# Performance work log

Hardware: AMD Instinct MI355X
Metric: run time of the kernel (lower is better)

Reference implementation:

```python
import jax, jax.numpy as jnp
import numpy as np

N_NODES = 100000
D_EMB = 128          # per-node embedding dim; concat dim = 2*D_EMB = 256
HIDDEN = 64
N_EDGES = 300000


def setup_inputs() -> dict:
    key = jax.random.key(0)
    ks = jax.random.split(key, 8)
    src_embs = jax.random.normal(ks[0], (N_NODES, D_EMB), dtype=jnp.float32)
    dst_embs = jax.random.normal(ks[1], (N_NODES, D_EMB), dtype=jnp.float32)
    edges_src_ids = jax.random.randint(ks[2], (N_EDGES,), 0, N_NODES, dtype=jnp.int64)
    edges_dst_ids = jax.random.randint(ks[3], (N_EDGES,), 0, N_NODES, dtype=jnp.int64)
    # elayers = Linear(256, 64) -> ReLU -> Linear(64, 1)
    s1 = 1.0 / np.sqrt(2 * D_EMB)
    s2 = 1.0 / np.sqrt(HIDDEN)
    W1 = jax.random.uniform(ks[4], (2 * D_EMB, HIDDEN), jnp.float32, -s1, s1)
    b1 = jax.random.uniform(ks[5], (HIDDEN,), jnp.float32, -s1, s1)
    W2 = jax.random.uniform(ks[6], (HIDDEN, 1), jnp.float32, -s2, s2)
    b2 = jax.random.uniform(ks[7], (1,), jnp.float32, -s2, s2)
    return {
        "src_embs": src_embs,
        "dst_embs": dst_embs,
        "edges_src_ids": edges_src_ids,
        "edges_dst_ids": edges_dst_ids,
        "W1": W1,
        "b1": b1,
        "W2": W2,
        "b2": b2,
    }


def reference(src_embs, dst_embs, edges_src_ids, edges_dst_ids, W1, b1, W2, b2):
    # Gather per-edge endpoint embeddings and concatenate: [E, 2*D]
    edge_feats = jnp.concatenate(
        [src_embs[edges_src_ids], dst_embs[edges_dst_ids]], axis=1
    )
    # Linear -> ReLU -> Linear, producing one logit per edge: [E, 1]
    h = jax.nn.relu(edge_feats @ W1 + b1)
    edge_logits = h @ W2 + b2
    return edge_logits
```

## Files before the change

kernel.cpp:

```cpp
#include <hip/hip_runtime.h>
#include <hip/hip_bf16.h>

typedef float f32x4 __attribute__((ext_vector_type(4)));
typedef __bf16 bf16x8 __attribute__((ext_vector_type(8)));
typedef __bf16 bf16x4 __attribute__((ext_vector_type(4)));

#define DEMB 128
#define HIDDEN 64
#define W1T_STRIDE 264

typedef const __attribute__((address_space(1))) void* gas_ptr;
typedef __attribute__((address_space(3))) void* las_ptr;

__global__ __launch_bounds__(256) void w1frag_kernel(
    const float* __restrict__ W1, __bf16* __restrict__ wsfrag)
{
    const int gid = blockIdx.x * 256 + threadIdx.x;
    if (gid >= 2048) return;
    const int tb  = gid >> 10;
    const int cid = gid & 1023;
    const int el = cid & 15;
    const int gk = (cid >> 4) & 3;
    const int kk = (cid >> 6) & 3;
    const int t  = (cid >> 8) & 3;
    const int kbase = tb * 128 + kk * 32 + gk * 8;
    bf16x8 ch;
#pragma unroll
    for (int j = 0; j < 8; ++j)
        ch[j] = (__bf16)W1[(kbase + j) * HIDDEN + 4 * el + t];
    *reinterpret_cast<bf16x8*>(wsfrag + (size_t)gid * 8) = ch;
}

__global__ __launch_bounds__(256) void node_part9_kernel(
    const float* __restrict__ src_embs,
    const float* __restrict__ dst_embs,
    const __bf16* __restrict__ wsfrag,
    __bf16* __restrict__ spart,
    __bf16* __restrict__ dpart,
    int n_tiles, int blocks_per_table)
{
    __shared__ __bf16 frag_lds[1024 * 8];
    __shared__ float  bounce[4][512];

    const int table = (blockIdx.x >= blocks_per_table) ? 1 : 0;
    const int bid = blockIdx.x - table * blocks_per_table;
    const float* __restrict__ E = table ? dst_embs : src_embs;
    __bf16* __restrict__ P = table ? dpart : spart;

    const int lane = threadIdx.x & 63;
    const int el = lane & 15;
    const int gk = lane >> 4;
    const int wid = threadIdx.x >> 6;

    {
        const char* src = (const char*)(wsfrag + (size_t)table * 1024 * 8);
#pragma unroll
        for (int r = 0; r < 4; ++r) {
            const int off = (wid * 4 + r) * 1024;
            __builtin_amdgcn_global_load_lds(
                (gas_ptr)(src + off + lane * 16),
                (las_ptr)((char*)frag_lds + off), 16, 0, 0);
        }
        asm volatile("s_waitcnt vmcnt(0)" ::: "memory");
    }
    __syncthreads();

    char* obc = (char*)&bounce[wid][0];
    const int tstride = blocks_per_table * 4;
    int tile = bid * 4 + wid;
    if (tile >= n_tiles) return;

    f32x4 Ra[8], Rb[8];

#define LOADT(T, R)                                                          \
    do {                                                                     \
        const float* rp_ = E + (size_t)(T) * 2048 + el * 128 + gk * 8;       \
        _Pragma("unroll")                                                    \
        for (int kk = 0; kk < 4; ++kk) {                                     \
            (R)[2 * kk]     = *reinterpret_cast<const f32x4*>(rp_ + kk * 32);\
            (R)[2 * kk + 1] = *reinterpret_cast<const f32x4*>(rp_ + kk * 32 + 4);\
        }                                                                    \
    } while (0)

#define COMPUTE_STORE(T, R)                                                  \
    do {                                                                     \
        f32x4 acc[4] = {{0.f,0.f,0.f,0.f},{0.f,0.f,0.f,0.f},                 \
                        {0.f,0.f,0.f,0.f},{0.f,0.f,0.f,0.f}};                \
        _Pragma("unroll")                                                    \
        for (int kk = 0; kk < 4; ++kk) {                                     \
            bf16x8 a;                                                        \
            _Pragma("unroll")                                                \
            for (int j = 0; j < 4; ++j) {                                    \
                a[j]     = (__bf16)(R)[2 * kk][j];                           \
                a[4 + j] = (__bf16)(R)[2 * kk + 1][j];                       \
            }                                                                \
            _Pragma("unroll")                                                \
            for (int t = 0; t < 4; ++t) {                                    \
                const bf16x8 b = *reinterpret_cast<const bf16x8*>(           \
                    &frag_lds[(size_t)((t * 4 + kk) * 4 + gk) * 128 + el * 8]);\
                acc[t] = __builtin_amdgcn_mfma_f32_16x16x32_bf16(a, b, acc[t], 0, 0, 0);\
            }                                                                \
        }                                                                    \
        _Pragma("unroll")                                                    \
        for (int r = 0; r < 4; ++r) {                                        \
            bf16x4 pk;                                                       \
            _Pragma("unroll")                                                \
            for (int t = 0; t < 4; ++t) pk[t] = (__bf16)acc[t][r];           \
            *reinterpret_cast<bf16x4*>(obc + (gk * 4 + r) * 128 + el * 8) = pk;\
        }                                                                    \
        asm volatile("s_waitcnt lgkmcnt(0)" ::: "memory");                   \
        f32x4 c0 = *reinterpret_cast<const f32x4*>(obc + lane * 32);         \
        f32x4 c1 = *reinterpret_cast<const f32x4*>(obc + lane * 32 + 16);    \
        char* pb = (char*)P + (size_t)(T) * 2048;                            \
        *reinterpret_cast<f32x4*>(pb + lane * 32) = c0;                      \
        *reinterpret_cast<f32x4*>(pb + lane * 32 + 16) = c1;                 \
    } while (0)

    LOADT(tile, Ra);
    bool useA = true;
    while (true) {
        const int nxt = tile + tstride;
        if (useA) {
            if (nxt < n_tiles) LOADT(nxt, Rb);
            __builtin_amdgcn_sched_barrier(0);
            COMPUTE_STORE(tile, Ra);
        } else {
            if (nxt < n_tiles) LOADT(nxt, Ra);
            __builtin_amdgcn_sched_barrier(0);
            COMPUTE_STORE(tile, Rb);
        }
        useA = !useA;
        tile = nxt;
        if (tile >= n_tiles) break;
    }
#undef LOADT
#undef COMPUTE_STORE
}

__global__ __launch_bounds__(256, 8) void edge_tail2_kernel(
    const __bf16* __restrict__ spart,
    const __bf16* __restrict__ dpart,
    const int* __restrict__ src_ids,
    const int* __restrict__ dst_ids,
    const float* __restrict__ b1,
    const float* __restrict__ W2,
    const float* __restrict__ b2,
    float* __restrict__ out,
    int n_edges)
{
    const int lane = threadIdx.x & 63;
    const int c = lane & 7;
    float b1v[8], w2v[8];
#pragma unroll
    for (int j = 0; j < 8; ++j) { b1v[j] = b1[c * 8 + j]; w2v[j] = W2[c * 8 + j]; }
    const float bias2 = b2[0];

    int gid = (blockIdx.x * blockDim.x + threadIdx.x) >> 3;
    const int gstride = (gridDim.x * blockDim.x) >> 3;

    for (int e = gid; e < n_edges; e += gstride) {
        const long long sid = src_ids[e];
        const long long did = dst_ids[e];
        const bf16x8 s8 = *reinterpret_cast<const bf16x8*>(spart + sid * HIDDEN + c * 8);
        const bf16x8 d8 = *reinterpret_cast<const bf16x8*>(dpart + did * HIDDEN + c * 8);
        float v = 0.f;
#pragma unroll
        for (int j = 0; j < 8; ++j) {
            float h = (float)s8[j] + (float)d8[j] + b1v[j];
            h = fmaxf(h, 0.f);
            v = fmaf(h, w2v[j], v);
        }
        v += __shfl_xor(v, 1, 64);
        v += __shfl_xor(v, 2, 64);
        v += __shfl_xor(v, 4, 64);
        if (c == 0) out[e] = v + bias2;
    }
}

__global__ __launch_bounds__(256) void edge_mlp_kernel(
    const float* __restrict__ src_embs,
    const float* __restrict__ dst_embs,
    const int* __restrict__ src_ids,
    const int* __restrict__ dst_ids,
    const float* __restrict__ W1,
    const float* __restrict__ b1,
    const float* __restrict__ W2,
    const float* __restrict__ b2,
    float* __restrict__ out,
    int n_edges, int n_groups)
{
    __shared__ __bf16 w1t[64 * W1T_STRIDE];
    for (int s = threadIdx.x; s < 256 * 64; s += 256) {
        int k = s >> 6;
        int n = s & 63;
        w1t[n * W1T_STRIDE + k] = (__bf16)W1[s];
    }
    __syncthreads();

    const int lane = threadIdx.x & 63;
    const int el = lane & 15;
    const int gk = lane >> 4;

    float b1v[4], w2v[4];
#pragma unroll
    for (int t = 0; t < 4; ++t) { b1v[t] = b1[16 * t + el]; w2v[t] = W2[16 * t + el]; }
    const float bias2 = b2[0];

    const int gw0 = blockIdx.x * 4 + (threadIdx.x >> 6);
    const int gstride = gridDim.x * 4;

    for (int g = gw0; g < n_groups; g += gstride) {
        const int e_base = g * 16;
        int e = e_base + el;
        if (e >= n_edges) e = n_edges - 1;
        const long long sid = src_ids[e];
        const long long did = dst_ids[e];
        const float* sp = src_embs + sid * DEMB + gk * 8;
        const float* dp = dst_embs + did * DEMB + gk * 8;

        f32x4 acc[4] = {{0.f,0.f,0.f,0.f},{0.f,0.f,0.f,0.f},
                        {0.f,0.f,0.f,0.f},{0.f,0.f,0.f,0.f}};
#pragma unroll
        for (int kk = 0; kk < 8; ++kk) {
            const float* ap = (kk < 4) ? (sp + kk * 32) : (dp + (kk - 4) * 32);
            f32x4 f0 = *reinterpret_cast<const f32x4*>(ap);
            f32x4 f1 = *reinterpret_cast<const f32x4*>(ap + 4);
            bf16x8 a;
#pragma unroll
            for (int j = 0; j < 4; ++j) { a[j] = (__bf16)f0[j]; a[4+j] = (__bf16)f1[j]; }
#pragma unroll
            for (int t = 0; t < 4; ++t) {
                const bf16x8 bfrag = *reinterpret_cast<const bf16x8*>(
                    &w1t[(16 * t + el) * W1T_STRIDE + kk * 32 + gk * 8]);
                acc[t] = __builtin_amdgcn_mfma_f32_16x16x32_bf16(a, bfrag, acc[t], 0, 0, 0);
            }
        }
        float s0[4];
#pragma unroll
        for (int r = 0; r < 4; ++r) {
            float v = 0.f;
#pragma unroll
            for (int t = 0; t < 4; ++t) {
                float h = acc[t][r] + b1v[t];
                h = fmaxf(h, 0.f);
                v = fmaf(h, w2v[t], v);
            }
#pragma unroll
            for (int m = 1; m < 16; m <<= 1) v += __shfl_xor(v, m, 64);
            s0[r] = v + bias2;
        }
        const int row0 = e_base + gk * 4;
        if (el == 0) {
            if (row0 + 4 <= n_edges) {
                f32x4 o = {s0[0], s0[1], s0[2], s0[3]};
                *reinterpret_cast<f32x4*>(out + row0) = o;
            } else {
#pragma unroll
                for (int r = 0; r < 4; ++r)
                    if (row0 + r < n_edges) out[row0 + r] = s0[r];
            }
        }
    }
}

extern "C" void kernel_launch(void* const* d_in, const int* in_sizes, int n_in,
                              void* d_out, int out_size, void* d_ws, size_t ws_size,
                              hipStream_t stream) {
    const float* src_embs = (const float*)d_in[0];
    const float* dst_embs = (const float*)d_in[1];
    const int*   src_ids  = (const int*)d_in[2];
    const int*   dst_ids  = (const int*)d_in[3];
    const float* W1 = (const float*)d_in[4];
    const float* b1 = (const float*)d_in[5];
    const float* W2 = (const float*)d_in[6];
    const float* b2 = (const float*)d_in[7];
    float* out = (float*)d_out;

    const int n_edges = in_sizes[2];
    const int n_nodes = in_sizes[0] / DEMB;
    const size_t part_elems = (size_t)n_nodes * HIDDEN;
    const size_t need = 2 * part_elems * sizeof(__bf16) + 32768;

    if (ws_size >= need && (n_nodes % 16) == 0) {
        __bf16* spart = (__bf16*)d_ws;
        __bf16* dpart = spart + part_elems;
        __bf16* wsfrag = dpart + part_elems;
        const int n_tiles = n_nodes / 16;

        w1frag_kernel<<<8, 256, 0, stream>>>(W1, wsfrag);

        int bpt = 384;
        if (bpt * 4 > n_tiles) bpt = (n_tiles + 3) / 4;
        node_part9_kernel<<<2 * bpt, 256, 0, stream>>>(
            src_embs, dst_embs, wsfrag, spart, dpart, n_tiles, bpt);

        int blocks2 = (n_edges + 31) / 32;
        if (blocks2 > 2048) blocks2 = 2048;
        edge_tail2_kernel<<<blocks2, 256, 0, stream>>>(
            spart, dpart, src_ids, dst_ids, b1, W2, b2, out, n_edges);
    } else {
        const int n_groups = (n_edges + 15) / 16;
        int blocks = (n_groups + 3) / 4;
        if (blocks > 1024) blocks = 1024;
        edge_mlp_kernel<<<blocks, 256, 0, stream>>>(
            src_embs, dst_embs, src_ids, dst_ids, W1, b1, W2, b2, out,
            n_edges, n_groups);
    }
}
```

Measured before the change: 43.34 us.

## Fuse W1 fragment prep into node kernel and triple-buffer tile loads

Removes the separate w1frag kernel launch: each block now converts its half of W1 to bf16 MFMA fragments directly into LDS. The node projection loop moves from double to triple buffering of embedding tiles, with out-of-range prefetches clamped to the last tile, and the grid drops from 384 to 256 blocks per table. This saves a launch and deepens prefetch, but every block now does redundant strided fp32 reads of W1, and the extra register buffer may lower occupancy.

```diff
diff --git a/kernel.cpp b/kernel.cpp
--- a/kernel.cpp
+++ b/kernel.cpp
@@ -9,32 +9,10 @@
 #define HIDDEN 64
 #define W1T_STRIDE 264
 
-typedef const __attribute__((address_space(1))) void* gas_ptr;
-typedef __attribute__((address_space(3))) void* las_ptr;
-
-__global__ __launch_bounds__(256) void w1frag_kernel(
-    const float* __restrict__ W1, __bf16* __restrict__ wsfrag)
-{
-    const int gid = blockIdx.x * 256 + threadIdx.x;
-    if (gid >= 2048) return;
-    const int tb  = gid >> 10;
-    const int cid = gid & 1023;
-    const int el = cid & 15;
-    const int gk = (cid >> 4) & 3;
-    const int kk = (cid >> 6) & 3;
-    const int t  = (cid >> 8) & 3;
-    const int kbase = tb * 128 + kk * 32 + gk * 8;
-    bf16x8 ch;
-#pragma unroll
-    for (int j = 0; j < 8; ++j)
-        ch[j] = (__bf16)W1[(kbase + j) * HIDDEN + 4 * el + t];
-    *reinterpret_cast<bf16x8*>(wsfrag + (size_t)gid * 8) = ch;
-}
-
-__global__ __launch_bounds__(256) void node_part9_kernel(
+__global__ void node_partB_kernel(
     const float* __restrict__ src_embs,
     const float* __restrict__ dst_embs,
-    const __bf16* __restrict__ wsfrag,
+    const float* __restrict__ W1,
     __bf16* __restrict__ spart,
     __bf16* __restrict__ dpart,
     int n_tiles, int blocks_per_table)
@@ -46,35 +24,38 @@
     const int bid = blockIdx.x - table * blocks_per_table;
     const float* __restrict__ E = table ? dst_embs : src_embs;
     __bf16* __restrict__ P = table ? dpart : spart;
+    const int kofs = table * 128;
+
+    for (int cid = threadIdx.x; cid < 1024; cid += 256) {
+        const int el = cid & 15;
+        const int gk = (cid >> 4) & 3;
+        const int kk = (cid >> 6) & 3;
+        const int t  = (cid >> 8) & 3;
+        const int kbase = kofs + kk * 32 + gk * 8;
+        bf16x8 ch;
+#pragma unroll
+        for (int j = 0; j < 8; ++j)
+            ch[j] = (__bf16)W1[(kbase + j) * HIDDEN + 4 * el + t];
+        *reinterpret_cast<bf16x8*>(&frag_lds[cid * 8]) = ch;
+    }
+    __syncthreads();
 
     const int lane = threadIdx.x & 63;
     const int el = lane & 15;
     const int gk = lane >> 4;
     const int wid = threadIdx.x >> 6;
-
-    {
-        const char* src = (const char*)(wsfrag + (size_t)table * 1024 * 8);
-#pragma unroll
-        for (int r = 0; r < 4; ++r) {
-            const int off = (wid * 4 + r) * 1024;
-            __builtin_amdgcn_global_load_lds(
-                (gas_ptr)(src + off + lane * 16),
-                (las_ptr)((char*)frag_lds + off), 16, 0, 0);
-        }
-        asm volatile("s_waitcnt vmcnt(0)" ::: "memory");
-    }
-    __syncthreads();
-
     char* obc = (char*)&bounce[wid][0];
-    const int tstride = blocks_per_table * 4;
+
+    const int ts = blocks_per_table * 4;
     int tile = bid * 4 + wid;
     if (tile >= n_tiles) return;
 
-    f32x4 Ra[8], Rb[8];
+    f32x4 Ra[8], Rb[8], Rc[8];
 
 #define LOADT(T, R)                                                          \
     do {                                                                     \
-        const float* rp_ = E + (size_t)(T) * 2048 + el * 128 + gk * 8;       \
+        int tc_ = (T); if (tc_ >= n_tiles) tc_ = n_tiles - 1;                \
+        const float* rp_ = E + (size_t)tc_ * 2048 + el * 128 + gk * 8;       \
         _Pragma("unroll")                                                    \
         for (int kk = 0; kk < 4; ++kk) {                                     \
             (R)[2 * kk]     = *reinterpret_cast<const f32x4*>(rp_ + kk * 32);\
@@ -109,6 +90,7 @@
             *reinterpret_cast<bf16x4*>(obc + (gk * 4 + r) * 128 + el * 8) = pk;\
         }                                                                    \
         asm volatile("s_waitcnt lgkmcnt(0)" ::: "memory");                   \
+        __builtin_amdgcn_sched_barrier(0);                                   \
         f32x4 c0 = *reinterpret_cast<const f32x4*>(obc + lane * 32);         \
         f32x4 c1 = *reinterpret_cast<const f32x4*>(obc + lane * 32 + 16);    \
         char* pb = (char*)P + (size_t)(T) * 2048;                            \
@@ -117,21 +99,23 @@
     } while (0)
 
     LOADT(tile, Ra);
-    bool useA = true;
+    LOADT(tile + ts, Rb);
+
     while (true) {
-        const int nxt = tile + tstride;
-        if (useA) {
-            if (nxt < n_tiles) LOADT(nxt, Rb);
-            __builtin_amdgcn_sched_barrier(0);
-            COMPUTE_STORE(tile, Ra);
-        } else {
-            if (nxt < n_tiles) LOADT(nxt, Ra);
-            __builtin_amdgcn_sched_barrier(0);
-            COMPUTE_STORE(tile, Rb);
-        }
-        useA = !useA;
-        tile = nxt;
-        if (tile >= n_tiles) break;
+        LOADT(tile + 2 * ts, Rc);
+        __builtin_amdgcn_sched_barrier(0);
+        COMPUTE_STORE(tile, Ra);
+        tile += ts; if (tile >= n_tiles) break;
+
+        LOADT(tile + 2 * ts, Ra);
+        __builtin_amdgcn_sched_barrier(0);
+        COMPUTE_STORE(tile, Rb);
+        tile += ts; if (tile >= n_tiles) break;
+
+        LOADT(tile + 2 * ts, Rb);
+        __builtin_amdgcn_sched_barrier(0);
+        COMPUTE_STORE(tile, Rc);
+        tile += ts; if (tile >= n_tiles) break;
     }
 #undef LOADT
 #undef COMPUTE_STORE
@@ -279,20 +263,17 @@
     const int n_edges = in_sizes[2];
     const int n_nodes = in_sizes[0] / DEMB;
     const size_t part_elems = (size_t)n_nodes * HIDDEN;
-    const size_t need = 2 * part_elems * sizeof(__bf16) + 32768;
+    const size_t need = 2 * part_elems * sizeof(__bf16);
 
     if (ws_size >= need && (n_nodes % 16) == 0) {
         __bf16* spart = (__bf16*)d_ws;
         __bf16* dpart = spart + part_elems;
-        __bf16* wsfrag = dpart + part_elems;
         const int n_tiles = n_nodes / 16;
 
-        w1frag_kernel<<<8, 256, 0, stream>>>(W1, wsfrag);
-
-        int bpt = 384;
+        int bpt = 256;
         if (bpt * 4 > n_tiles) bpt = (n_tiles + 3) / 4;
-        node_part9_kernel<<<2 * bpt, 256, 0, stream>>>(
-            src_embs, dst_embs, wsfrag, spart, dpart, n_tiles, bpt);
+        node_partB_kernel<<<2 * bpt, 256, 0, stream>>>(
+            src_embs, dst_embs, W1, spart, dpart, n_tiles, bpt);
 
         int blocks2 = (n_edges + 31) / 32;
         if (blocks2 > 2048) blocks2 = 2048;
```

Measured after the change: 44.42 us. 2.5% more time.
